# Kernel optimization log

Hardware: AMD Instinct MI355X
Metric: run time of the kernel (lower is better)

## Reference

```python
import jax, jax.numpy as jnp
import numpy as np

V, S, E, H, D, L = 32000, 1024, 512, 8, 64, 4
FF = 4 * E
EPS = 1e-5


def setup_inputs() -> dict:
    key = jax.random.key(0)
    ks = jax.random.split(key, 24)
    s = 0.02
    inp = {
        "x": jax.random.randint(ks[0], (2, S), 0, V, dtype=jnp.int32),
        "tok_emb": jax.random.normal(ks[1], (V, E), jnp.float32) * s,
        "pos_emb": jax.random.normal(ks[2], (S, E), jnp.float32) * s,
        "Wq": jax.random.normal(ks[3], (L, H, E, D), jnp.float32) * s,
        "bq": jnp.zeros((L, H, D), jnp.float32),
        "Wk": jax.random.normal(ks[4], (L, H, E, D), jnp.float32) * s,
        "bk": jnp.zeros((L, H, D), jnp.float32),
        "Wv": jax.random.normal(ks[5], (L, H, E, D), jnp.float32) * s,
        "bv": jnp.zeros((L, H, D), jnp.float32),
        "Wo": jax.random.normal(ks[6], (L, H * D, E), jnp.float32) * s,
        "bo": jnp.zeros((L, E), jnp.float32),
        "W1": jax.random.normal(ks[7], (L, E, FF), jnp.float32) * s,
        "b1": jnp.zeros((L, FF), jnp.float32),
        "W2": jax.random.normal(ks[8], (L, FF, E), jnp.float32) * s,
        "b2": jnp.zeros((L, E), jnp.float32),
        "ln1_g": jnp.ones((L, E), jnp.float32),
        "ln1_b": jnp.zeros((L, E), jnp.float32),
        "ln2_g": jnp.ones((L, E), jnp.float32),
        "ln2_b": jnp.zeros((L, E), jnp.float32),
        "Wout": jax.random.normal(ks[9], (E, V), jnp.float32) * s,
        "bout": jnp.zeros((V,), jnp.float32),
    }
    return inp


def _layernorm(x, g, b):
    mu = jnp.mean(x, axis=-1, keepdims=True)
    var = jnp.mean(jnp.square(x - mu), axis=-1, keepdims=True)
    return (x - mu) * jax.lax.rsqrt(var + EPS) * g + b


def _decoder(h, Wq, bq, Wk, bk, Wv, bv, Wo, bo, W1, b1, W2, b2, g1, be1, g2, be2):
    B, T, _ = h.shape
    # per-head Q/K/V projections, batched over heads (matches concat of per-head linears)
    Q = jnp.einsum("bse,hed->bhsd", h, Wq) + bq[None, :, None, :]
    K = jnp.einsum("bse,hed->bhsd", h, Wk) + bk[None, :, None, :]
    Vv = jnp.einsum("bse,hed->bhsd", h, Wv) + bv[None, :, None, :]
    scores = jnp.einsum("bhqd,bhkd->bhqk", Q, K) / jnp.sqrt(jnp.asarray(D, h.dtype))
    causal = jnp.tril(jnp.ones((T, T), bool))
    scores = jnp.where(causal[None, None], scores, -jnp.inf)
    attn = jax.nn.softmax(scores, axis=-1)
    out = jnp.einsum("bhqk,bhkd->bhqd", attn, Vv)
    conc = out.transpose(0, 2, 1, 3).reshape(B, T, H * D)  # concat heads along feature dim
    mha = conc @ Wo + bo
    ln = _layernorm(h + mha, g1, be1)
    ff = jax.nn.relu(ln @ W1 + b1) @ W2 + b2
    return _layernorm(ln + ff, g2, be2)


def reference(x, tok_emb, pos_emb, Wq, bq, Wk, bk, Wv, bv, Wo, bo,
              W1, b1, W2, b2, ln1_g, ln1_b, ln2_g, ln2_b, Wout, bout):
    B, T = x.shape
    h = tok_emb[x] + pos_emb[:T][None]  # [B,T,E]
    for l in range(L):
        h = _decoder(h, Wq[l], bq[l], Wk[l], bk[l], Wv[l], bv[l], Wo[l], bo[l],
                     W1[l], b1[l], W2[l], b2[l], ln1_g[l], ln1_b[l], ln2_g[l], ln2_b[l])
    return h @ Wout + bout  # [B,T,V] logits
```

## Files before the change

### kernel.cpp

```cpp
#include <hip/hip_runtime.h>
#include <hip/hip_bf16.h>


#define B_ 2
#define S_ 1024
#define E_ 512
#define H_ 8
#define D_ 64
#define L_ 4
#define FF_ 2048
#define V_ 32000
#define M_ (B_ * S_)
#define QKV_N (3 * H_ * D_)

typedef __attribute__((ext_vector_type(8))) short short8;
typedef __attribute__((ext_vector_type(8))) ushort ushort8;
typedef __attribute__((ext_vector_type(4))) float f32x4;

__device__ __forceinline__ float b2f(ushort u) {
  union { uint32_t i; float f; } c; c.i = ((uint32_t)u) << 16; return c.f;
}
__device__ __forceinline__ ushort f2b(float f) {
  union { float f; uint32_t i; } c; c.f = f;
  uint32_t u = c.i;
  return (ushort)((u + 0x7FFFu + ((u >> 16) & 1u)) >> 16);
}

__device__ __forceinline__ void gload16(const ushort* g, ushort* l) {
  __builtin_amdgcn_global_load_lds(
      (const __attribute__((address_space(1))) void*)g,
      (__attribute__((address_space(3))) void*)l, 16, 0, 0);
}

__global__ __launch_bounds__(256) void setup_kernel(
    const int* __restrict__ x, const float* __restrict__ tok,
    const float* __restrict__ pos, float* __restrict__ hf, ushort* __restrict__ hb,
    const float* __restrict__ Wq, const float* __restrict__ Wk,
    const float* __restrict__ Wv, ushort* __restrict__ wqkv,
    const float* __restrict__ Wo, ushort* __restrict__ wo_t,
    const float* __restrict__ W1, ushort* __restrict__ w1_t,
    const float* __restrict__ W2, ushort* __restrict__ w2_t,
    const float* __restrict__ Wout, ushort* __restrict__ wout_t,
    const float* __restrict__ bq, const float* __restrict__ bk,
    const float* __restrict__ bv, float* __restrict__ bqkv) {
  __shared__ float tile[32][33];
  int bz = blockIdx.x;
  int tid = threadIdx.x;

  auto tr32 = [&](const float* in, ushort* out, int inC, int R, int r0, int c0) {
    int tx = tid & 31, ty = tid >> 5;
#pragma unroll
    for (int i = 0; i < 4; i++)
      tile[ty + 8 * i][tx] = in[(size_t)(r0 + ty + 8 * i) * inC + c0 + tx];
    __syncthreads();
#pragma unroll
    for (int i = 0; i < 4; i++)
      out[(size_t)(c0 + ty + 8 * i) * R + r0 + tx] = f2b(tile[tx][ty + 8 * i]);
  };

  if (bz < 4096) {
    int idx = bz * 256 + tid;
    int e = idx & (E_ - 1);
    int t = (idx >> 9) & (S_ - 1);
    int b = idx >> 19;
    int tokid = x[b * S_ + t];
    float v = tok[(size_t)tokid * E_ + e] + pos[(size_t)t * E_ + e];
    hf[idx] = v;
    hb[idx] = f2b(v);
  } else if (bz < 7168) {
    int li = bz - 4096;
    int batch = li >> 5, q = li & 31;
    int t = batch / (L_ * H_);
    int rem = batch % (L_ * H_);
    int lyr = rem / H_, h = rem % H_;
    const float* in = ((t == 0) ? Wq : (t == 1) ? Wk : Wv) +
                      ((size_t)lyr * H_ + h) * E_ * D_;
    ushort* out = wqkv + (size_t)lyr * QKV_N * E_ + ((size_t)t * 512 + h * 64) * E_;
    tr32(in, out, D_, E_, (q & 15) * 32, (q >> 4) * 32);
  } else if (bz < 8192) {
    int li = bz - 7168;
    int lyr = li >> 8, q = li & 255;
    tr32(Wo + (size_t)lyr * E_ * E_, wo_t + (size_t)lyr * E_ * E_, E_, E_,
         (q & 15) * 32, (q >> 4) * 32);
  } else if (bz < 12288) {
    int li = bz - 8192;
    int lyr = li >> 10, q = li & 1023;
    tr32(W1 + (size_t)lyr * E_ * FF_, w1_t + (size_t)lyr * FF_ * E_, FF_, E_,
         (q & 15) * 32, (q >> 4) * 32);
  } else if (bz < 16384) {
    int li = bz - 12288;
    int lyr = li >> 10, q = li & 1023;
    tr32(W2 + (size_t)lyr * FF_ * E_, w2_t + (size_t)lyr * E_ * FF_, E_, FF_,
         (q & 63) * 32, (q >> 6) * 32);
  } else if (bz < 32384) {
    int li = bz - 16384;
    tr32(Wout, wout_t, V_, E_, (li & 15) * 32, (li >> 4) * 32);
  } else {
    int idx = (bz - 32384) * 256 + tid;
    if (idx < L_ * QKV_N) {
      int n = idx % QKV_N;
      int lyr = idx / QKV_N;
      int t = n / (H_ * D_);
      int hd = n % (H_ * D_);
      const float* src = (t == 0) ? bq : (t == 1) ? bk : bv;
      bqkv[idx] = src[(size_t)lyr * H_ * D_ + hd];
    }
  }
}

template <bool OUTBF, bool RELU, bool VT>
__global__ __launch_bounds__(256) void mfma_gemm_kernel(
    const ushort* __restrict__ A, const ushort* __restrict__ Bt,
    const float* __restrict__ bias, const float* __restrict__ resid,
    void* __restrict__ out, ushort* __restrict__ vt,
    int M, int N, int K, int gx) {
  __shared__ __align__(16) ushort As[128 * 64];
  __shared__ __align__(16) ushort Bs[128 * 64];
  int tid = threadIdx.x;
  int w = tid >> 6, l = tid & 63;
  int wr = w >> 1, wc = w & 1;
  int lane15 = l & 15, lhi = l >> 4;

  int bid = blockIdx.x;
  int bx = bid % gx, by = bid / gx;
  int row0 = by * 128, col0 = bx * 128;

  int rr8 = l >> 3;
  int ksrc = (((l & 7) ^ rr8) << 3);
  const ushort *gA[2][2], *gB[2][2];
  ushort *lA[2][2], *lB[2][2];
#pragma unroll
  for (int cc = 0; cc < 2; cc++) {
    int c = w + cc * 4;
#pragma unroll
    for (int h = 0; h < 2; h++) {
      int row = c * 16 + h * 8 + rr8;
      gA[cc][h] = A + (size_t)(row0 + row) * K + ksrc;
      gB[cc][h] = Bt + (size_t)(col0 + row) * K + ksrc;
      int ldst = c * 1024 + h * 512 + l * 8;
      lA[cc][h] = &As[ldst];
      lB[cc][h] = &Bs[ldst];
    }
  }

  f32x4 acc[4][4] = {};

  for (int k0 = 0; k0 < K; k0 += 64) {
#pragma unroll
    for (int cc = 0; cc < 2; cc++)
#pragma unroll
      for (int h = 0; h < 2; h++) {
        gload16(gA[cc][h] + k0, lA[cc][h]);
        gload16(gB[cc][h] + k0, lB[cc][h]);
      }
    __syncthreads();
    short8 a[4][2], b[4][2];
    int sa = (lane15 & 7) << 4;
#pragma unroll
    for (int i = 0; i < 4; i++) {
      int ra = (wr * 64 + i * 16 + lane15) * 64;
      int rb = (wc * 64 + i * 16 + lane15) * 64;
#pragma unroll
      for (int kk = 0; kk < 2; kk++) {
        int inner = ((kk * 64 + lhi * 16) ^ sa) >> 1;
        a[i][kk] = *(const short8*)&As[ra + inner];
        b[i][kk] = *(const short8*)&Bs[rb + inner];
      }
    }
#pragma unroll
    for (int i = 0; i < 4; i++)
#pragma unroll
      for (int j = 0; j < 4; j++) {
        acc[i][j] = __builtin_amdgcn_mfma_f32_16x16x32_bf16(a[i][0], b[j][0], acc[i][j], 0, 0, 0);
        acc[i][j] = __builtin_amdgcn_mfma_f32_16x16x32_bf16(a[i][1], b[j][1], acc[i][j], 0, 0, 0);
      }
    __syncthreads();
  }

  float* outf = (float*)out;
  ushort* outb = (ushort*)out;
#pragma unroll
  for (int i = 0; i < 4; i++) {
    int gr = row0 + wr * 64 + i * 16 + lhi * 4;
#pragma unroll
    for (int j = 0; j < 4; j++) {
      int gc = col0 + wc * 64 + j * 16 + lane15;
      float bb = bias[gc];
#pragma unroll
      for (int r = 0; r < 4; r++) {
        float v = acc[i][j][r] + bb;
        if (resid) v += resid[(size_t)(gr + r) * N + gc];
        if (RELU) v = fmaxf(v, 0.f);
        if (VT && gc >= 1024) {
          int d = gc - 1024;
          int grr = gr + r;
          int bb2 = grr >> 10, s = grr & 1023;
          vt[(((size_t)(bb2 * 8 + (d >> 6)) * 64 + (d & 63)) << 10) + s] = f2b(v);
        } else if (OUTBF) {
          outb[(size_t)(gr + r) * N + gc] = f2b(v);
        } else {
          outf[(size_t)(gr + r) * N + gc] = v;
        }
      }
    }
  }
}

template <int SK>
__global__ __launch_bounds__(256) void mfma_gemm_sk_kernel(
    const ushort* __restrict__ A, const ushort* __restrict__ Bt,
    ushort* __restrict__ part, int M, int N, int K, int gx) {
  __shared__ __align__(16) ushort As[128 * 64];
  __shared__ __align__(16) ushort Bs[128 * 64];
  int tid = threadIdx.x;
  int w = tid >> 6, l = tid & 63;
  int wr = w >> 1, wc = w & 1;
  int lane15 = l & 15, lhi = l >> 4;

  int tiles = gx * (M >> 7);
  int sk = blockIdx.x / tiles;
  int rem = blockIdx.x % tiles;
  int bx = rem % gx, by = rem / gx;
  int row0 = by * 128, col0 = bx * 128;
  int klen = K / SK, kbeg = sk * klen;

  int rr8 = l >> 3;
  int ksrc = (((l & 7) ^ rr8) << 3);
  const ushort *gA[2][2], *gB[2][2];
  ushort *lA[2][2], *lB[2][2];
#pragma unroll
  for (int cc = 0; cc < 2; cc++) {
    int c = w + cc * 4;
#pragma unroll
    for (int h = 0; h < 2; h++) {
      int row = c * 16 + h * 8 + rr8;
      gA[cc][h] = A + (size_t)(row0 + row) * K + ksrc;
      gB[cc][h] = Bt + (size_t)(col0 + row) * K + ksrc;
      int ldst = c * 1024 + h * 512 + l * 8;
      lA[cc][h] = &As[ldst];
      lB[cc][h] = &Bs[ldst];
    }
  }

  f32x4 acc[4][4] = {};

  for (int k0 = kbeg; k0 < kbeg + klen; k0 += 64) {
#pragma unroll
    for (int cc = 0; cc < 2; cc++)
#pragma unroll
      for (int h = 0; h < 2; h++) {
        gload16(gA[cc][h] + k0, lA[cc][h]);
        gload16(gB[cc][h] + k0, lB[cc][h]);
      }
    __syncthreads();
    short8 a[4][2], b[4][2];
    int sa = (lane15 & 7) << 4;
#pragma unroll
    for (int i = 0; i < 4; i++) {
      int ra = (wr * 64 + i * 16 + lane15) * 64;
      int rb = (wc * 64 + i * 16 + lane15) * 64;
#pragma unroll
      for (int kk = 0; kk < 2; kk++) {
        int inner = ((kk * 64 + lhi * 16) ^ sa) >> 1;
        a[i][kk] = *(const short8*)&As[ra + inner];
        b[i][kk] = *(const short8*)&Bs[rb + inner];
      }
    }
#pragma unroll
    for (int i = 0; i < 4; i++)
#pragma unroll
      for (int j = 0; j < 4; j++) {
        acc[i][j] = __builtin_amdgcn_mfma_f32_16x16x32_bf16(a[i][0], b[j][0], acc[i][j], 0, 0, 0);
        acc[i][j] = __builtin_amdgcn_mfma_f32_16x16x32_bf16(a[i][1], b[j][1], acc[i][j], 0, 0, 0);
      }
    __syncthreads();
  }

  ushort* dst = part + (size_t)sk * M * N;
#pragma unroll
  for (int i = 0; i < 4; i++) {
    int gr = row0 + wr * 64 + i * 16 + lhi * 4;
#pragma unroll
    for (int j = 0; j < 4; j++) {
      int gc = col0 + wc * 64 + j * 16 + lane15;
#pragma unroll
      for (int r = 0; r < 4; r++)
        dst[(size_t)(gr + r) * N + gc] = f2b(acc[i][j][r]);
    }
  }
}

__global__ __launch_bounds__(512) void gemm_fin_kernel(
    const ushort* __restrict__ A, const ushort* __restrict__ Bt,
    const float* __restrict__ bias, float* __restrict__ out) {
  constexpr int K = E_, N = V_, NT = E_ / 64;
  __shared__ __align__(16) ushort As[2][128 * 64];
  __shared__ __align__(16) ushort Bs[3][256 * 64];
  int tid = threadIdx.x;
  int w = tid >> 6, l = tid & 63;
  int wr = w >> 2, wc = w & 3;
  int lane15 = l & 15, lhi = l >> 4;

  int bid = blockIdx.x;
  int wg = (bid & 7) * 250 + (bid >> 3);
  int by = wg & 15, bx = wg >> 4;
  int row0 = by * 128, col0 = bx * 256;

  const ushort* ga[2]; int la[2];
  const ushort* gb[4]; int lb[4];
#pragma unroll
  for (int p = 0; p < 2; p++) {
    int i = p * 512 + tid;
    int row = i >> 3, kg = i & 7;
    ga[p] = A + (size_t)(row0 + row) * K + ((kg ^ (row & 7)) << 3);
    la[p] = i * 8;
  }
#pragma unroll
  for (int p = 0; p < 4; p++) {
    int i = p * 512 + tid;
    int row = i >> 3, kg = i & 7;
    gb[p] = Bt + (size_t)(col0 + row) * K + ((kg ^ (row & 7)) << 3);
    lb[p] = i * 8;
  }

  f32x4 acc[4][4] = {};

  auto stageA = [&](int buf, int t) {
    int k0 = t << 6;
#pragma unroll
    for (int p = 0; p < 2; p++) gload16(ga[p] + k0, &As[buf][la[p]]);
  };
  auto stageB = [&](int buf, int t) {
    int k0 = t << 6;
#pragma unroll
    for (int p = 0; p < 4; p++) gload16(gb[p] + k0, &Bs[buf][lb[p]]);
  };
  auto compute = [&](int ba, int bb) {
    int sa = (lane15 & 7) << 4;
#pragma unroll
    for (int kk = 0; kk < 2; kk++) {
      int inner = ((kk * 64 + lhi * 16) ^ sa) >> 1;
      short8 a[4], b[4];
#pragma unroll
      for (int i = 0; i < 4; i++)
        a[i] = *(const short8*)&As[ba][(wr * 64 + i * 16 + lane15) * 64 + inner];
#pragma unroll
      for (int j = 0; j < 4; j++)
        b[j] = *(const short8*)&Bs[bb][(wc * 64 + j * 16 + lane15) * 64 + inner];
#pragma unroll
      for (int i = 0; i < 4; i++)
#pragma unroll
        for (int j = 0; j < 4; j++)
          acc[i][j] = __builtin_amdgcn_mfma_f32_16x16x32_bf16(a[i], b[j], acc[i][j], 0, 0, 0);
    }
  };

  stageA(0, 0);
  stageB(0, 0);
  stageB(1, 1);
  __builtin_amdgcn_sched_barrier(0);
  asm volatile("s_waitcnt vmcnt(4)" ::: "memory");
  __builtin_amdgcn_s_barrier();
  __builtin_amdgcn_sched_barrier(0);

#pragma unroll
  for (int t = 0; t < NT; t++) {
    if (t + 1 < NT) stageA((t + 1) & 1, t + 1);
    if (t + 2 < NT) stageB((t + 2) % 3, t + 2);
    __builtin_amdgcn_s_setprio(1);
    compute(t & 1, t % 3);
    __builtin_amdgcn_s_setprio(0);
    if (t + 1 < NT) {
      __builtin_amdgcn_sched_barrier(0);
      if (t + 2 < NT) asm volatile("s_waitcnt vmcnt(4)" ::: "memory");
      else            asm volatile("s_waitcnt vmcnt(0)" ::: "memory");
      __builtin_amdgcn_s_barrier();
      __builtin_amdgcn_sched_barrier(0);
    }
  }

#pragma unroll
  for (int i = 0; i < 4; i++) {
    int gr = row0 + wr * 64 + i * 16 + lhi * 4;
#pragma unroll
    for (int j = 0; j < 4; j++) {
      int gc = col0 + wc * 64 + j * 16 + lane15;
      float bb = bias[gc];
#pragma unroll
      for (int r = 0; r < 4; r++)
        out[(size_t)(gr + r) * N + gc] = acc[i][j][r] + bb;
    }
  }
}

__global__ __launch_bounds__(128) void fattn_kernel(
    const ushort* __restrict__ qkv, const ushort* __restrict__ vt,
    ushort* __restrict__ conc) {
  int qb = blockIdx.x;
  int bh = blockIdx.y;
  int b = bh >> 3, h = bh & 7;
  int w = threadIdx.x >> 6, l = threadIdx.x & 63;
  int lane15 = l & 15, lhi = l >> 4;
  int q0 = qb * 32 + w * 16;

  __shared__ __align__(16) ushort plds[2][16][72];

  const ushort* qr = qkv + (size_t)(b * S_ + q0 + lane15) * QKV_N + h * 64;
  short8 qf0 = *(const short8*)(qr + lhi * 8);
  short8 qf1 = *(const short8*)(qr + 32 + lhi * 8);

  f32x4 o[4] = {};
  float lsum[4] = {0.f, 0.f, 0.f, 0.f};

  const ushort* kbase = qkv + (size_t)b * S_ * QKV_N + 512 + h * 64;
  const ushort* vbase = vt + (size_t)bh * 64 * S_;
  int qtop = q0 + 15;

  for (int kv0 = 0; kv0 <= qtop; kv0 += 64) {
#pragma unroll
    for (int r = 0; r < 4; r++) {
    }
    float pr[4][4];
#pragma unroll
    for (int t = 0; t < 4; t++) {
      if (kv0 + t * 16 <= qtop) {
        const ushort* kr = kbase + (size_t)(kv0 + t * 16 + lane15) * QKV_N;
        short8 kf0 = *(const short8*)(kr + lhi * 8);
        short8 kf1 = *(const short8*)(kr + 32 + lhi * 8);
        f32x4 s = {};
        s = __builtin_amdgcn_mfma_f32_16x16x32_bf16(qf0, kf0, s, 0, 0, 0);
        s = __builtin_amdgcn_mfma_f32_16x16x32_bf16(qf1, kf1, s, 0, 0, 0);
        int kidx = kv0 + t * 16 + lane15;
#pragma unroll
        for (int r = 0; r < 4; r++) {
          float p = (kidx > q0 + lhi * 4 + r) ? 0.f : __expf(s[r] * 0.125f);
          pr[t][r] = p;
          plds[w][lhi * 4 + r][t * 16 + lane15] = f2b(p);
        }
      } else {
#pragma unroll
        for (int r = 0; r < 4; r++) {
          pr[t][r] = 0.f;
          plds[w][lhi * 4 + r][t * 16 + lane15] = 0;
        }
      }
    }
#pragma unroll
    for (int r = 0; r < 4; r++) {
      float rs = (pr[0][r] + pr[1][r]) + (pr[2][r] + pr[3][r]);
      rs += __shfl_xor(rs, 1);
      rs += __shfl_xor(rs, 2);
      rs += __shfl_xor(rs, 4);
      rs += __shfl_xor(rs, 8);
      lsum[r] += rs;
    }
    short8 pa0 = *(const short8*)&plds[w][lane15][lhi * 8];
    short8 pa1 = *(const short8*)&plds[w][lane15][32 + lhi * 8];
#pragma unroll
    for (int n = 0; n < 4; n++) {
      const ushort* vr = vbase + (size_t)(n * 16 + lane15) * S_ + kv0;
      short8 vf0 = *(const short8*)(vr + lhi * 8);
      short8 vf1 = *(const short8*)(vr + 32 + lhi * 8);
      o[n] = __builtin_amdgcn_mfma_f32_16x16x32_bf16(pa0, vf0, o[n], 0, 0, 0);
      o[n] = __builtin_amdgcn_mfma_f32_16x16x32_bf16(pa1, vf1, o[n], 0, 0, 0);
    }
  }
#pragma unroll
  for (int r = 0; r < 4; r++) {
    float inv = 1.f / lsum[r];
    int row = b * S_ + q0 + lhi * 4 + r;
#pragma unroll
    for (int n = 0; n < 4; n++)
      conc[(size_t)row * (H_ * D_) + h * 64 + n * 16 + lane15] = f2b(o[n][r] * inv);
  }
}

template <int SK>
__global__ __launch_bounds__(256) void ln_red_kernel(
    const ushort* __restrict__ part, const float* __restrict__ bias,
    const float* __restrict__ resid, const float* __restrict__ g,
    const float* __restrict__ bsh, float* __restrict__ outf,
    ushort* __restrict__ outb) {
  int w = threadIdx.x >> 6, l = threadIdx.x & 63;
  int row = blockIdx.x * 4 + w;
  size_t off = (size_t)row * E_ + l * 8;
  float4 r0 = *(const float4*)(resid + off);
  float4 r1 = *(const float4*)(resid + off + 4);
  float4 bb0 = *(const float4*)(bias + l * 8);
  float4 bb1 = *(const float4*)(bias + l * 8 + 4);
  float x[8] = {r0.x + bb0.x, r0.y + bb0.y, r0.z + bb0.z, r0.w + bb0.w,
                r1.x + bb1.x, r1.y + bb1.y, r1.z + bb1.z, r1.w + bb1.w};
#pragma unroll
  for (int s = 0; s < SK; s++) {
    ushort8 pv = *(const ushort8*)(part + (size_t)s * M_ * E_ + off);
#pragma unroll
    for (int i = 0; i < 8; i++) x[i] += b2f(pv[i]);
  }
  float s = 0.f, q = 0.f;
#pragma unroll
  for (int i = 0; i < 8; i++) { s += x[i]; q += x[i] * x[i]; }
#pragma unroll
  for (int off2 = 1; off2 < 64; off2 <<= 1) {
    s += __shfl_xor(s, off2);
    q += __shfl_xor(q, off2);
  }
  float mu = s * (1.f / 512.f);
  float var = q * (1.f / 512.f) - mu * mu;
  float rs = rsqrtf(var + 1e-5f);
  float4 g0 = *(const float4*)(g + l * 8);
  float4 g1 = *(const float4*)(g + l * 8 + 4);
  float4 b0 = *(const float4*)(bsh + l * 8);
  float4 b1 = *(const float4*)(bsh + l * 8 + 4);
  float gg[8] = {g0.x, g0.y, g0.z, g0.w, g1.x, g1.y, g1.z, g1.w};
  float bbv[8] = {b0.x, b0.y, b0.z, b0.w, b1.x, b1.y, b1.z, b1.w};
  float y[8];
#pragma unroll
  for (int i = 0; i < 8; i++) y[i] = (x[i] - mu) * rs * gg[i] + bbv[i];
  float* of = outf + off;
  *(float4*)of = make_float4(y[0], y[1], y[2], y[3]);
  *(float4*)(of + 4) = make_float4(y[4], y[5], y[6], y[7]);
  ushort4 u0 = {f2b(y[0]), f2b(y[1]), f2b(y[2]), f2b(y[3])};
  ushort4 u1 = {f2b(y[4]), f2b(y[5]), f2b(y[6]), f2b(y[7])};
  ushort* ob = outb + off;
  *(ushort4*)ob = u0;
  *(ushort4*)(ob + 4) = u1;
}

extern "C" void kernel_launch(void* const* d_in, const int* in_sizes, int n_in,
                              void* d_out, int out_size, void* d_ws, size_t ws_size,
                              hipStream_t stream) {
  const int* x = (const int*)d_in[0];
  const float* tok = (const float*)d_in[1];
  const float* pos = (const float*)d_in[2];
  const float* Wq = (const float*)d_in[3];
  const float* bq = (const float*)d_in[4];
  const float* Wk = (const float*)d_in[5];
  const float* bk = (const float*)d_in[6];
  const float* Wv = (const float*)d_in[7];
  const float* bv = (const float*)d_in[8];
  const float* Wo = (const float*)d_in[9];
  const float* bo = (const float*)d_in[10];
  const float* W1 = (const float*)d_in[11];
  const float* b1 = (const float*)d_in[12];
  const float* W2 = (const float*)d_in[13];
  const float* b2 = (const float*)d_in[14];
  const float* ln1g = (const float*)d_in[15];
  const float* ln1b = (const float*)d_in[16];
  const float* ln2g = (const float*)d_in[17];
  const float* ln2b = (const float*)d_in[18];
  const float* Wout = (const float*)d_in[19];
  const float* bout = (const float*)d_in[20];
  float* out = (float*)d_out;

  char* p = (char*)d_ws;
  auto alloc = [&](size_t bytes) {
    char* r = p;
    p += (bytes + 255) & ~(size_t)255;
    return r;
  };
  float* h_f = (float*)alloc((size_t)M_ * E_ * 4);
  ushort* h_b = (ushort*)alloc((size_t)M_ * E_ * 2);
  ushort* qkv_b = (ushort*)alloc((size_t)M_ * QKV_N * 2);
  ushort* conc_b = (ushort*)alloc((size_t)M_ * E_ * 2);
  ushort* part = (ushort*)alloc((size_t)4 * M_ * E_ * 2);
  float* ln_f = (float*)alloc((size_t)M_ * E_ * 4);
  ushort* ln_b = (ushort*)alloc((size_t)M_ * E_ * 2);
  ushort* ff_b = (ushort*)alloc((size_t)M_ * FF_ * 2);
  ushort* vt_b = (ushort*)alloc((size_t)B_ * H_ * D_ * S_ * 2);
  ushort* wqkv = (ushort*)alloc((size_t)L_ * QKV_N * E_ * 2);
  float* bqkv = (float*)alloc((size_t)L_ * QKV_N * 4);
  ushort* wo_t = (ushort*)alloc((size_t)L_ * E_ * E_ * 2);
  ushort* w1_t = (ushort*)alloc((size_t)L_ * FF_ * E_ * 2);
  ushort* w2_t = (ushort*)alloc((size_t)L_ * E_ * FF_ * 2);
  ushort* wout_t = (ushort*)alloc((size_t)V_ * E_ * 2);

  setup_kernel<<<32408, 256, 0, stream>>>(
      x, tok, pos, h_f, h_b, Wq, Wk, Wv, wqkv, Wo, wo_t, W1, w1_t,
      W2, w2_t, Wout, wout_t, bq, bk, bv, bqkv);

  for (int l = 0; l < L_; ++l) {
    mfma_gemm_kernel<true, false, true><<<(QKV_N / 128) * (M_ / 128), 256, 0, stream>>>(
        h_b, wqkv + (size_t)l * QKV_N * E_, bqkv + l * QKV_N, nullptr,
        qkv_b, vt_b, M_, QKV_N, E_, QKV_N / 128);
    fattn_kernel<<<dim3(S_ / 32, B_ * H_), 128, 0, stream>>>(qkv_b, vt_b, conc_b);
    mfma_gemm_sk_kernel<4><<<4 * (E_ / 128) * (M_ / 128), 256, 0, stream>>>(
        conc_b, wo_t + (size_t)l * E_ * E_, part, M_, E_, E_, E_ / 128);
    ln_red_kernel<4><<<M_ / 4, 256, 0, stream>>>(
        part, bo + l * E_, h_f, ln1g + l * E_, ln1b + l * E_, ln_f, ln_b);
    mfma_gemm_kernel<true, true, false><<<(FF_ / 128) * (M_ / 128), 256, 0, stream>>>(
        ln_b, w1_t + (size_t)l * FF_ * E_, b1 + l * FF_, nullptr, ff_b, nullptr,
        M_, FF_, E_, FF_ / 128);
    mfma_gemm_sk_kernel<4><<<4 * (E_ / 128) * (M_ / 128), 256, 0, stream>>>(
        ff_b, w2_t + (size_t)l * E_ * FF_, part, M_, E_, FF_, E_ / 128);
    ln_red_kernel<4><<<M_ / 4, 256, 0, stream>>>(
        part, b2 + l * E_, ln_f, ln2g + l * E_, ln2b + l * E_, h_f, h_b);
  }

  gemm_fin_kernel<<<(M_ / 128) * (V_ / 256), 512, 0, stream>>>(
      h_b, wout_t, bout, out);
}
```

Baseline: 614.1 us.

## Double-buffer GEMM LDS tiles and balance causal attention across query tiles

The MFMA GEMM and split-K GEMM kernels now double-buffer their shared-memory tiles. The next K-slice is prefetched while the current one is computed, with explicit vmcnt waits, barriers and priority raising. This is meant to hide global-load latency that the single-buffer loop with two syncthreads exposed. The attention kernel switches to single-wave blocks, each handling a short query tile and its mirror tile (qb and 63-qb) to even out causal work per block. The trade-offs are doubled LDS use, which can cut occupancy, and a hand-tuned vmcnt count that depends on gload16 issuing exactly the expected number of loads.

```diff
diff --git a/kernel.cpp b/kernel.cpp
--- a/kernel.cpp
+++ b/kernel.cpp
@@ -114,8 +114,8 @@
     const float* __restrict__ bias, const float* __restrict__ resid,
     void* __restrict__ out, ushort* __restrict__ vt,
     int M, int N, int K, int gx) {
-  __shared__ __align__(16) ushort As[128 * 64];
-  __shared__ __align__(16) ushort Bs[128 * 64];
+  __shared__ __align__(16) ushort As[2 * 8192];
+  __shared__ __align__(16) ushort Bs[2 * 8192];
   int tid = threadIdx.x;
   int w = tid >> 6, l = tid & 63;
   int wr = w >> 1, wc = w & 1;
@@ -128,7 +128,7 @@
   int rr8 = l >> 3;
   int ksrc = (((l & 7) ^ rr8) << 3);
   const ushort *gA[2][2], *gB[2][2];
-  ushort *lA[2][2], *lB[2][2];
+  int lofs[2][2];
 #pragma unroll
   for (int cc = 0; cc < 2; cc++) {
     int c = w + cc * 4;
@@ -137,29 +137,32 @@
       int row = c * 16 + h * 8 + rr8;
       gA[cc][h] = A + (size_t)(row0 + row) * K + ksrc;
       gB[cc][h] = Bt + (size_t)(col0 + row) * K + ksrc;
-      int ldst = c * 1024 + h * 512 + l * 8;
-      lA[cc][h] = &As[ldst];
-      lB[cc][h] = &Bs[ldst];
+      lofs[cc][h] = c * 1024 + h * 512 + l * 8;
     }
   }
 
   f32x4 acc[4][4] = {};
-
-  for (int k0 = 0; k0 < K; k0 += 64) {
+  int nt = K >> 6;
+
+  auto stage = [&](int buf, int t) {
+    int k0 = t << 6;
+    int ob = buf << 13;
 #pragma unroll
     for (int cc = 0; cc < 2; cc++)
 #pragma unroll
       for (int h = 0; h < 2; h++) {
-        gload16(gA[cc][h] + k0, lA[cc][h]);
-        gload16(gB[cc][h] + k0, lB[cc][h]);
-      }
-    __syncthreads();
+        gload16(gA[cc][h] + k0, &As[ob + lofs[cc][h]]);
+        gload16(gB[cc][h] + k0, &Bs[ob + lofs[cc][h]]);
+      }
+  };
+  auto compute = [&](int buf) {
+    int ob = buf << 13;
+    int sa = (lane15 & 7) << 4;
     short8 a[4][2], b[4][2];
-    int sa = (lane15 & 7) << 4;
 #pragma unroll
     for (int i = 0; i < 4; i++) {
-      int ra = (wr * 64 + i * 16 + lane15) * 64;
-      int rb = (wc * 64 + i * 16 + lane15) * 64;
+      int ra = ob + (wr * 64 + i * 16 + lane15) * 64;
+      int rb = ob + (wc * 64 + i * 16 + lane15) * 64;
 #pragma unroll
       for (int kk = 0; kk < 2; kk++) {
         int inner = ((kk * 64 + lhi * 16) ^ sa) >> 1;
@@ -174,7 +177,25 @@
         acc[i][j] = __builtin_amdgcn_mfma_f32_16x16x32_bf16(a[i][0], b[j][0], acc[i][j], 0, 0, 0);
         acc[i][j] = __builtin_amdgcn_mfma_f32_16x16x32_bf16(a[i][1], b[j][1], acc[i][j], 0, 0, 0);
       }
-    __syncthreads();
+  };
+
+  stage(0, 0);
+  for (int t = 0; t < nt; t++) {
+    if (t + 1 < nt) {
+      stage((t + 1) & 1, t + 1);
+      __builtin_amdgcn_sched_barrier(0);
+      asm volatile("s_waitcnt vmcnt(8)" ::: "memory");
+    } else {
+      __builtin_amdgcn_sched_barrier(0);
+      asm volatile("s_waitcnt vmcnt(0)" ::: "memory");
+    }
+    __builtin_amdgcn_s_barrier();
+    __builtin_amdgcn_sched_barrier(0);
+    __builtin_amdgcn_s_setprio(1);
+    compute(t & 1);
+    __builtin_amdgcn_s_setprio(0);
+    __builtin_amdgcn_sched_barrier(0);
+    __builtin_amdgcn_s_barrier();
   }
 
   float* outf = (float*)out;
@@ -210,8 +231,8 @@
 __global__ __launch_bounds__(256) void mfma_gemm_sk_kernel(
     const ushort* __restrict__ A, const ushort* __restrict__ Bt,
     ushort* __restrict__ part, int M, int N, int K, int gx) {
-  __shared__ __align__(16) ushort As[128 * 64];
-  __shared__ __align__(16) ushort Bs[128 * 64];
+  __shared__ __align__(16) ushort As[2 * 8192];
+  __shared__ __align__(16) ushort Bs[2 * 8192];
   int tid = threadIdx.x;
   int w = tid >> 6, l = tid & 63;
   int wr = w >> 1, wc = w & 1;
@@ -227,38 +248,41 @@
   int rr8 = l >> 3;
   int ksrc = (((l & 7) ^ rr8) << 3);
   const ushort *gA[2][2], *gB[2][2];
-  ushort *lA[2][2], *lB[2][2];
+  int lofs[2][2];
 #pragma unroll
   for (int cc = 0; cc < 2; cc++) {
     int c = w + cc * 4;
 #pragma unroll
     for (int h = 0; h < 2; h++) {
       int row = c * 16 + h * 8 + rr8;
-      gA[cc][h] = A + (size_t)(row0 + row) * K + ksrc;
-      gB[cc][h] = Bt + (size_t)(col0 + row) * K + ksrc;
-      int ldst = c * 1024 + h * 512 + l * 8;
-      lA[cc][h] = &As[ldst];
-      lB[cc][h] = &Bs[ldst];
+      gA[cc][h] = A + (size_t)(row0 + row) * K + kbeg + ksrc;
+      gB[cc][h] = Bt + (size_t)(col0 + row) * K + kbeg + ksrc;
+      lofs[cc][h] = c * 1024 + h * 512 + l * 8;
     }
   }
 
   f32x4 acc[4][4] = {};
-
-  for (int k0 = kbeg; k0 < kbeg + klen; k0 += 64) {
+  int nt = klen >> 6;
+
+  auto stage = [&](int buf, int t) {
+    int k0 = t << 6;
+    int ob = buf << 13;
 #pragma unroll
     for (int cc = 0; cc < 2; cc++)
 #pragma unroll
       for (int h = 0; h < 2; h++) {
-        gload16(gA[cc][h] + k0, lA[cc][h]);
-        gload16(gB[cc][h] + k0, lB[cc][h]);
-      }
-    __syncthreads();
+        gload16(gA[cc][h] + k0, &As[ob + lofs[cc][h]]);
+        gload16(gB[cc][h] + k0, &Bs[ob + lofs[cc][h]]);
+      }
+  };
+  auto compute = [&](int buf) {
+    int ob = buf << 13;
+    int sa = (lane15 & 7) << 4;
     short8 a[4][2], b[4][2];
-    int sa = (lane15 & 7) << 4;
 #pragma unroll
     for (int i = 0; i < 4; i++) {
-      int ra = (wr * 64 + i * 16 + lane15) * 64;
-      int rb = (wc * 64 + i * 16 + lane15) * 64;
+      int ra = ob + (wr * 64 + i * 16 + lane15) * 64;
+      int rb = ob + (wc * 64 + i * 16 + lane15) * 64;
 #pragma unroll
       for (int kk = 0; kk < 2; kk++) {
         int inner = ((kk * 64 + lhi * 16) ^ sa) >> 1;
@@ -273,7 +297,25 @@
         acc[i][j] = __builtin_amdgcn_mfma_f32_16x16x32_bf16(a[i][0], b[j][0], acc[i][j], 0, 0, 0);
         acc[i][j] = __builtin_amdgcn_mfma_f32_16x16x32_bf16(a[i][1], b[j][1], acc[i][j], 0, 0, 0);
       }
-    __syncthreads();
+  };
+
+  stage(0, 0);
+  for (int t = 0; t < nt; t++) {
+    if (t + 1 < nt) {
+      stage((t + 1) & 1, t + 1);
+      __builtin_amdgcn_sched_barrier(0);
+      asm volatile("s_waitcnt vmcnt(8)" ::: "memory");
+    } else {
+      __builtin_amdgcn_sched_barrier(0);
+      asm volatile("s_waitcnt vmcnt(0)" ::: "memory");
+    }
+    __builtin_amdgcn_s_barrier();
+    __builtin_amdgcn_sched_barrier(0);
+    __builtin_amdgcn_s_setprio(1);
+    compute(t & 1);
+    __builtin_amdgcn_s_setprio(0);
+    __builtin_amdgcn_sched_barrier(0);
+    __builtin_amdgcn_s_barrier();
   }
 
   ushort* dst = part + (size_t)sk * M * N;
@@ -393,85 +435,87 @@
   }
 }
 
-__global__ __launch_bounds__(128) void fattn_kernel(
+__global__ __launch_bounds__(64) void fattn_kernel(
     const ushort* __restrict__ qkv, const ushort* __restrict__ vt,
     ushort* __restrict__ conc) {
   int qb = blockIdx.x;
   int bh = blockIdx.y;
   int b = bh >> 3, h = bh & 7;
-  int w = threadIdx.x >> 6, l = threadIdx.x & 63;
+  int l = threadIdx.x;
   int lane15 = l & 15, lhi = l >> 4;
-  int q0 = qb * 32 + w * 16;
-
-  __shared__ __align__(16) ushort plds[2][16][72];
-
-  const ushort* qr = qkv + (size_t)(b * S_ + q0 + lane15) * QKV_N + h * 64;
-  short8 qf0 = *(const short8*)(qr + lhi * 8);
-  short8 qf1 = *(const short8*)(qr + 32 + lhi * 8);
-
-  f32x4 o[4] = {};
-  float lsum[4] = {0.f, 0.f, 0.f, 0.f};
+
+  __shared__ __align__(16) ushort plds[16][72];
 
   const ushort* kbase = qkv + (size_t)b * S_ * QKV_N + 512 + h * 64;
   const ushort* vbase = vt + (size_t)bh * 64 * S_;
-  int qtop = q0 + 15;
-
-  for (int kv0 = 0; kv0 <= qtop; kv0 += 64) {
+
+#pragma unroll
+  for (int pass = 0; pass < 2; pass++) {
+    int tile = pass ? (63 - qb) : qb;
+    int q0 = tile * 16;
+    int qtop = q0 + 15;
+
+    const ushort* qr = qkv + (size_t)(b * S_ + q0 + lane15) * QKV_N + h * 64;
+    short8 qf0 = *(const short8*)(qr + lhi * 8);
+    short8 qf1 = *(const short8*)(qr + 32 + lhi * 8);
+
+    f32x4 o[4] = {};
+    float lsum[4] = {0.f, 0.f, 0.f, 0.f};
+
+    for (int kv0 = 0; kv0 <= qtop; kv0 += 64) {
+      float pr[4][4];
+#pragma unroll
+      for (int t = 0; t < 4; t++) {
+        if (kv0 + t * 16 <= qtop) {
+          const ushort* kr = kbase + (size_t)(kv0 + t * 16 + lane15) * QKV_N;
+          short8 kf0 = *(const short8*)(kr + lhi * 8);
+          short8 kf1 = *(const short8*)(kr + 32 + lhi * 8);
+          f32x4 s = {};
+          s = __builtin_amdgcn_mfma_f32_16x16x32_bf16(qf0, kf0, s, 0, 0, 0);
+          s = __builtin_amdgcn_mfma_f32_16x16x32_bf16(qf1, kf1, s, 0, 0, 0);
+          int kidx = kv0 + t * 16 + lane15;
+#pragma unroll
+          for (int r = 0; r < 4; r++) {
+            float p = (kidx > q0 + lhi * 4 + r) ? 0.f : __expf(s[r] * 0.125f);
+            pr[t][r] = p;
+            plds[lhi * 4 + r][t * 16 + lane15] = f2b(p);
+          }
+        } else {
+#pragma unroll
+          for (int r = 0; r < 4; r++) {
+            pr[t][r] = 0.f;
+            plds[lhi * 4 + r][t * 16 + lane15] = 0;
+          }
+        }
+      }
+#pragma unroll
+      for (int r = 0; r < 4; r++) {
+        float rs = (pr[0][r] + pr[1][r]) + (pr[2][r] + pr[3][r]);
+        rs += __shfl_xor(rs, 1);
+        rs += __shfl_xor(rs, 2);
+        rs += __shfl_xor(rs, 4);
+        rs += __shfl_xor(rs, 8);
+        lsum[r] += rs;
+      }
+      short8 pa0 = *(const short8*)&plds[lane15][lhi * 8];
+      short8 pa1 = *(const short8*)&plds[lane15][32 + lhi * 8];
+#pragma unroll
+      for (int n = 0; n < 4; n++) {
+        const ushort* vr = vbase + (size_t)(n * 16 + lane15) * S_ + kv0;
+        short8 vf0 = *(const short8*)(vr + lhi * 8);
+        short8 vf1 = *(const short8*)(vr + 32 + lhi * 8);
+        o[n] = __builtin_amdgcn_mfma_f32_16x16x32_bf16(pa0, vf0, o[n], 0, 0, 0);
+        o[n] = __builtin_amdgcn_mfma_f32_16x16x32_bf16(pa1, vf1, o[n], 0, 0, 0);
+      }
+    }
 #pragma unroll
     for (int r = 0; r < 4; r++) {
-    }
-    float pr[4][4];
-#pragma unroll
-    for (int t = 0; t < 4; t++) {
-      if (kv0 + t * 16 <= qtop) {
-        const ushort* kr = kbase + (size_t)(kv0 + t * 16 + lane15) * QKV_N;
-        short8 kf0 = *(const short8*)(kr + lhi * 8);
-        short8 kf1 = *(const short8*)(kr + 32 + lhi * 8);
-        f32x4 s = {};
-        s = __builtin_amdgcn_mfma_f32_16x16x32_bf16(qf0, kf0, s, 0, 0, 0);
-        s = __builtin_amdgcn_mfma_f32_16x16x32_bf16(qf1, kf1, s, 0, 0, 0);
-        int kidx = kv0 + t * 16 + lane15;
-#pragma unroll
-        for (int r = 0; r < 4; r++) {
-          float p = (kidx > q0 + lhi * 4 + r) ? 0.f : __expf(s[r] * 0.125f);
-          pr[t][r] = p;
-          plds[w][lhi * 4 + r][t * 16 + lane15] = f2b(p);
-        }
-      } else {
-#pragma unroll
-        for (int r = 0; r < 4; r++) {
-          pr[t][r] = 0.f;
-          plds[w][lhi * 4 + r][t * 16 + lane15] = 0;
-        }
-      }
-    }
-#pragma unroll
-    for (int r = 0; r < 4; r++) {
-      float rs = (pr[0][r] + pr[1][r]) + (pr[2][r] + pr[3][r]);
-      rs += __shfl_xor(rs, 1);
-      rs += __shfl_xor(rs, 2);
-      rs += __shfl_xor(rs, 4);
-      rs += __shfl_xor(rs, 8);
-      lsum[r] += rs;
-    }
-    short8 pa0 = *(const short8*)&plds[w][lane15][lhi * 8];
-    short8 pa1 = *(const short8*)&plds[w][lane15][32 + lhi * 8];
-#pragma unroll
-    for (int n = 0; n < 4; n++) {
-      const ushort* vr = vbase + (size_t)(n * 16 + lane15) * S_ + kv0;
-      short8 vf0 = *(const short8*)(vr + lhi * 8);
-      short8 vf1 = *(const short8*)(vr + 32 + lhi * 8);
-      o[n] = __builtin_amdgcn_mfma_f32_16x16x32_bf16(pa0, vf0, o[n], 0, 0, 0);
-      o[n] = __builtin_amdgcn_mfma_f32_16x16x32_bf16(pa1, vf1, o[n], 0, 0, 0);
-    }
-  }
-#pragma unroll
-  for (int r = 0; r < 4; r++) {
-    float inv = 1.f / lsum[r];
-    int row = b * S_ + q0 + lhi * 4 + r;
-#pragma unroll
-    for (int n = 0; n < 4; n++)
-      conc[(size_t)row * (H_ * D_) + h * 64 + n * 16 + lane15] = f2b(o[n][r] * inv);
+      float inv = 1.f / lsum[r];
+      int row = b * S_ + q0 + lhi * 4 + r;
+#pragma unroll
+      for (int n = 0; n < 4; n++)
+        conc[(size_t)row * (H_ * D_) + h * 64 + n * 16 + lane15] = f2b(o[n][r] * inv);
+    }
   }
 }
 
@@ -582,7 +626,7 @@
     mfma_gemm_kernel<true, false, true><<<(QKV_N / 128) * (M_ / 128), 256, 0, stream>>>(
         h_b, wqkv + (size_t)l * QKV_N * E_, bqkv + l * QKV_N, nullptr,
         qkv_b, vt_b, M_, QKV_N, E_, QKV_N / 128);
-    fattn_kernel<<<dim3(S_ / 32, B_ * H_), 128, 0, stream>>>(qkv_b, vt_b, conc_b);
+    fattn_kernel<<<dim3(S_ / 32, B_ * H_), 64, 0, stream>>>(qkv_b, vt_b, conc_b);
     mfma_gemm_sk_kernel<4><<<4 * (E_ / 128) * (M_ / 128), 256, 0, stream>>>(
         conc_b, wo_t + (size_t)l * E_ * E_, part, M_, E_, E_, E_ / 128);
     ln_red_kernel<4><<<M_ / 4, 256, 0, stream>>>(
```

Measured after the change: 574.4 us. -6.5%, faster.
